# Kernel optimization log

Hardware: AMD Instinct MI355X
Metric: run time of the kernel (lower is better)

## Reference

```python
import jax, jax.numpy as jnp
import numpy as np

GROUPS = 32
EPS = 1e-6


def group_norm(x, gamma, beta):
    # x: [b, c, h, w], normalize over (c//GROUPS, h, w) within each group
    b, c, h, w = x.shape
    xg = x.reshape(b, GROUPS, c // GROUPS, h, w)
    mu = xg.mean(axis=(2, 3, 4), keepdims=True)
    var = xg.var(axis=(2, 3, 4), keepdims=True)
    xn = ((xg - mu) * jax.lax.rsqrt(var + EPS)).reshape(b, c, h, w)
    return xn * gamma[None, :, None, None] + beta[None, :, None, None]


def conv1x1(x, W, b):
    # 1x1 conv == channel GEMM. W: [out_c, in_c]
    return jnp.einsum('bchw,oc->bohw', x, W) + b[None, :, None, None]


def setup_inputs() -> dict:
    key = jax.random.key(0)
    ks = jax.random.split(key, 4)
    B, C, H, W = 4, 512, 64, 64
    wscale = 0.02
    return {
        'x': jax.random.normal(ks[0], (B, C, H, W), dtype=jnp.float32),
        'gn_w': jnp.ones((C,), dtype=jnp.float32),
        'gn_b': jnp.zeros((C,), dtype=jnp.float32),
        'q_w': jax.random.normal(ks[1], (C, C), dtype=jnp.float32) * wscale,
        'q_b': jnp.zeros((C,), dtype=jnp.float32),
        'k_w': jax.random.normal(ks[2], (C, C), dtype=jnp.float32) * wscale,
        'k_b': jnp.zeros((C,), dtype=jnp.float32),
        'v_w': jax.random.normal(ks[3], (C, C), dtype=jnp.float32) * wscale,
        'v_b': jnp.zeros((C,), dtype=jnp.float32),
    }


def reference(x, gn_w, gn_b, q_w, q_b, k_w, k_b, v_w, v_b):
    h_ = group_norm(x, gn_w, gn_b)
    q = conv1x1(h_, q_w, q_b)
    k = conv1x1(h_, k_w, k_b)
    v = conv1x1(h_, v_w, v_b)
    b, c, h, w = q.shape
    hw = h * w
    qf = q.reshape(b, c, hw)
    kf = k.reshape(b, c, hw)
    vf = v.reshape(b, c, hw)
    # attn[b, i, j] = sum_c q[b, c, i] * k[b, c, j] / sqrt(c)
    attn = jnp.einsum('bci,bcj->bij', qf, kf) * (c ** -0.5)
    attn = jax.nn.softmax(attn, axis=2)
    # A[b, c, i] = sum_j v[b, c, j] * attn[b, i, j]  (== bmm(v, attn^T))
    A = jnp.einsum('bcj,bij->bci', vf, attn).reshape(b, c, h, w)
    return x + A
```

## Files before the change

### kernel.cpp

```cpp
#include <hip/hip_runtime.h>
#include <hip/hip_bf16.h>

typedef __hip_bfloat16 bf16;
typedef __attribute__((ext_vector_type(8))) short short8;
typedef __attribute__((ext_vector_type(4))) float f32x4;
typedef __attribute__((ext_vector_type(8))) unsigned short u16x8;
typedef __attribute__((ext_vector_type(4))) unsigned short u16x4;

#define HWSZ 4096
#define CH 512
#define BATCH 4
#define NGROUPS 32
#define CPG 16
#define PER ((size_t)CH * HWSZ)

#define GLL16(gp, lp)                                                         \
  __builtin_amdgcn_global_load_lds(                                           \
      (const __attribute__((address_space(1))) void*)(gp),                    \
      (__attribute__((address_space(3))) void*)(lp), 16, 0, 0)

__device__ __forceinline__ float b2f(bf16 v) { return __bfloat162float(v); }
__device__ __forceinline__ bf16 f2b(float v) { return __float2bfloat16(v); }

__global__ void gn_part_kernel(const float* __restrict__ x, float2* __restrict__ gpart) {
  int bg = blockIdx.x >> 3, chunk = blockIdx.x & 7;
  size_t base = (size_t)bg * (CPG * HWSZ) + (size_t)chunk * 8192;
  int tid = threadIdx.x;
  float s = 0.f, ss = 0.f;
  const float4* xp = (const float4*)(x + base);
#pragma unroll
  for (int it = 0; it < 8; ++it) {
    float4 v = xp[tid + it * 256];
    s += v.x + v.y + v.z + v.w;
    ss += v.x * v.x + v.y * v.y + v.z * v.z + v.w * v.w;
  }
  __shared__ float rs[256], rss[256];
  rs[tid] = s; rss[tid] = ss;
  __syncthreads();
  for (int off = 128; off > 0; off >>= 1) {
    if (tid < off) { rs[tid] += rs[tid + off]; rss[tid] += rss[tid + off]; }
    __syncthreads();
  }
  if (tid == 0) gpart[blockIdx.x] = make_float2(rs[0], rss[0]);
}

__global__ void gn_final_kernel(const float2* __restrict__ gpart,
                                const float* __restrict__ gw, const float* __restrict__ gb,
                                float* __restrict__ sca, float* __restrict__ shf) {
  int idx = blockIdx.x * 256 + threadIdx.x;
  int b = idx >> 9, c = idx & 511;
  int bg = b * NGROUPS + (c >> 4);
  float s = 0.f, ss = 0.f;
#pragma unroll
  for (int t = 0; t < 8; ++t) {
    float2 p = gpart[bg * 8 + t];
    s += p.x; ss += p.y;
  }
  const float N = (float)(CPG * HWSZ);
  float mu = s / N;
  float var = ss / N - mu * mu;
  float inv = rsqrtf(var + 1e-6f);
  float a = inv * gw[c];
  sca[idx] = a;
  shf[idx] = gb[c] - mu * a;
}

__global__ void wconv_kernel(const float* __restrict__ qw, const float* __restrict__ kw,
                             const float* __restrict__ vw,
                             bf16* __restrict__ wq, bf16* __restrict__ wk, bf16* __restrict__ wv) {
  int i = blockIdx.x * 256 + threadIdx.x;
  wq[i] = f2b(qw[i]);
  wk[i] = f2b(kw[i]);
  wv[i] = f2b(vw[i]);
}

__global__ void h_apply_kernel(const float* __restrict__ x, const float* __restrict__ sca,
                               const float* __restrict__ shf, bf16* __restrict__ hT, int b0) {
  int p0 = blockIdx.x * 64, c0 = blockIdx.y * 64;
  int b = b0 + blockIdx.z;
  bf16* hTb = hT + (size_t)blockIdx.z * PER;
  __shared__ bf16 lt[64][66];
  int t = threadIdx.x;
  int pp = (t & 15) * 4, ccb = t >> 4;
#pragma unroll
  for (int it = 0; it < 4; ++it) {
    int cc = ccb + it * 16;
    int c = c0 + cc;
    float a = sca[b * CH + c], s = shf[b * CH + c];
    const float4 xv = *(const float4*)(x + ((size_t)(b * CH + c)) * HWSZ + p0 + pp);
    lt[cc][pp] = f2b(a * xv.x + s);
    lt[cc][pp + 1] = f2b(a * xv.y + s);
    lt[cc][pp + 2] = f2b(a * xv.z + s);
    lt[cc][pp + 3] = f2b(a * xv.w + s);
  }
  __syncthreads();
  int cc = (t & 15) * 4;
#pragma unroll
  for (int it = 0; it < 4; ++it) {
    int pr = (t >> 4) + it * 16;
    u16x4 o;
#pragma unroll
    for (int j = 0; j < 4; ++j) o[j] = *(const unsigned short*)&lt[cc + j][pr];
    *(u16x4*)(hTb + (size_t)(p0 + pr) * CH + c0 + cc) = o;
  }
}


__device__ __forceinline__ void mm_step(const bf16* la, const bf16* lb,
                                        f32x4 acc[4][4], int wm, int wn,
                                        int quad, int tm) {
#pragma unroll
  for (int kk = 0; kk < 2; ++kk) {
    const int go = ((kk * 4 + quad) ^ (tm & 7)) * 8;
    short8 aF[4], bF[4];
#pragma unroll
    for (int mt = 0; mt < 4; ++mt) {
      aF[mt] = *(const short8*)(la + (wm + mt * 16 + tm) * 64 + go);
      bF[mt] = *(const short8*)(lb + (wn + mt * 16 + tm) * 64 + go);
    }
#pragma unroll
    for (int mt = 0; mt < 4; ++mt)
#pragma unroll
      for (int nt = 0; nt < 4; ++nt)
        acc[mt][nt] = __builtin_amdgcn_mfma_f32_16x16x32_bf16(aF[mt], bF[nt],
                                                              acc[mt][nt], 0, 0, 0);
  }
}

#define MFMA_VARS()                                   \
  int tid = threadIdx.x;                              \
  int l = tid & 63, w = tid >> 6;                     \
  int quad = l >> 4, tm = l & 15;                     \
  int wm = (w & 1) * 64, wn = (w >> 1) * 64;          \
  int rr = l >> 3;                                    \
  int swz = ((l & 7) ^ rr) * 8;                       \
  bf16* stbase = smem + w * 2048

#define MSTAGE(bufsel, koff)                          \
  do {                                                \
    bf16* _d = stbase + (bufsel) * 16384;             \
    GLL16(sA0 + (koff), _d);                          \
    GLL16(sA1 + (koff), _d + 512);                    \
    GLL16(sA2 + (koff), _d + 1024);                   \
    GLL16(sA3 + (koff), _d + 1536);                   \
    GLL16(sB0 + (koff), _d + 8192);                   \
    GLL16(sB1 + (koff), _d + 8704);                   \
    GLL16(sB2 + (koff), _d + 9216);                   \
    GLL16(sB3 + (koff), _d + 9728);                   \
  } while (0)

#define MKLOOP(NS)                                                       \
  do {                                                                   \
    MSTAGE(0, 0);                                                        \
    for (int _t = 0; _t < (NS); ++_t) {                                  \
      if (_t + 1 < (NS)) {                                               \
        MSTAGE((_t + 1) & 1, (_t + 1) * 64);                             \
        asm volatile("s_waitcnt vmcnt(8)" ::: "memory");                 \
      } else {                                                           \
        asm volatile("s_waitcnt vmcnt(0)" ::: "memory");                 \
      }                                                                  \
      __builtin_amdgcn_s_barrier();                                      \
      mm_step(smem + (_t & 1) * 16384, smem + (_t & 1) * 16384 + 8192,   \
              acc, wm, wn, quad, tm);                                    \
      __builtin_amdgcn_s_barrier();                                      \
    }                                                                    \
  } while (0)

__global__ __launch_bounds__(256) void qkv_mfma(const bf16* __restrict__ hT,
                                                const bf16* __restrict__ wq,
                                                const bf16* __restrict__ wk,
                                                const bf16* __restrict__ wv,
                                                const float* __restrict__ qb,
                                                const float* __restrict__ kb,
                                                const float* __restrict__ vb,
                                                bf16* __restrict__ qT, bf16* __restrict__ kT,
                                                bf16* __restrict__ v) {
  int p0 = blockIdx.x * 128;
  int o0 = blockIdx.y * 128;
  int bz = blockIdx.z / 3, z = blockIdx.z % 3;
  const bf16* W = z == 0 ? wq : (z == 1 ? wk : wv);
  const float* bias = z == 0 ? qb : (z == 1 ? kb : vb);
  const bf16* hTb = hT + (size_t)bz * PER;
  __shared__ __align__(16) bf16 smem[32768];
  MFMA_VARS();
  const bf16* sA0 = hTb + (size_t)(p0 + w * 32 + rr) * CH + swz;
  const bf16* sA1 = sA0 + (size_t)8 * CH;
  const bf16* sA2 = sA0 + (size_t)16 * CH;
  const bf16* sA3 = sA0 + (size_t)24 * CH;
  const bf16* sB0 = W + (size_t)(o0 + w * 32 + rr) * CH + swz;
  const bf16* sB1 = sB0 + (size_t)8 * CH;
  const bf16* sB2 = sB0 + (size_t)16 * CH;
  const bf16* sB3 = sB0 + (size_t)24 * CH;
  f32x4 acc[4][4] = {};
  MKLOOP(CH / 64);
  if (z < 2) {
    bf16* outT = (z == 0 ? qT : kT) + (size_t)bz * PER;
#pragma unroll
    for (int nt = 0; nt < 4; ++nt) {
      int o = o0 + wn + nt * 16 + tm;
      float bv = bias[o];
#pragma unroll
      for (int mt = 0; mt < 4; ++mt)
#pragma unroll
        for (int r = 0; r < 4; ++r) {
          int p = p0 + wm + mt * 16 + quad * 4 + r;
          outT[(size_t)p * CH + o] = f2b(acc[mt][nt][r] + bv);
        }
    }
  } else {
    bf16* vv = v + (size_t)bz * PER;
    bf16* lt = smem;
    for (int chunk = 0; chunk < 2; ++chunk) {
      __syncthreads();
      if (wn == chunk * 64) {
#pragma unroll
        for (int nt = 0; nt < 4; ++nt) {
          int o = o0 + wn + nt * 16 + tm;
          float bv = bias[o];
#pragma unroll
          for (int mt = 0; mt < 4; ++mt)
#pragma unroll
            for (int r = 0; r < 4; ++r)
              lt[(nt * 16 + tm) * 136 + wm + mt * 16 + quad * 4 + r] = f2b(acc[mt][nt][r] + bv);
        }
      }
      __syncthreads();
      int oo = tid >> 2, ppb = (tid & 3) * 32;
      bf16* dst = vv + (size_t)(o0 + chunk * 64 + oo) * HWSZ + p0 + ppb;
      const bf16* src = lt + oo * 136 + ppb;
#pragma unroll
      for (int q4 = 0; q4 < 4; ++q4)
        *(u16x8*)(dst + q4 * 8) = *(const u16x8*)(src + q4 * 8);
    }
  }
}

__global__ __launch_bounds__(256) void s_mfma(const bf16* __restrict__ qT,
                                              const bf16* __restrict__ kT,
                                              bf16* __restrict__ attn,
                                              float* __restrict__ lsum) {
  int j0 = blockIdx.x * 128;
  int il0 = blockIdx.y * 128;
  int bz = blockIdx.z;
  const bf16* qTb = qT + (size_t)bz * PER;
  const bf16* kTb = kT + (size_t)bz * PER;
  bf16* attnb = attn + (size_t)bz * HWSZ * HWSZ;
  float* lsumb = lsum + (size_t)bz * HWSZ;
  __shared__ __align__(16) bf16 smem[32768];
  MFMA_VARS();
  const bf16* sA0 = qTb + (size_t)(il0 + w * 32 + rr) * CH + swz;
  const bf16* sA1 = sA0 + (size_t)8 * CH;
  const bf16* sA2 = sA0 + (size_t)16 * CH;
  const bf16* sA3 = sA0 + (size_t)24 * CH;
  const bf16* sB0 = kTb + (size_t)(j0 + w * 32 + rr) * CH + swz;
  const bf16* sB1 = sB0 + (size_t)8 * CH;
  const bf16* sB2 = sB0 + (size_t)16 * CH;
  const bf16* sB3 = sB0 + (size_t)24 * CH;
  f32x4 acc[4][4] = {};
  MKLOOP(CH / 64);
  const float scale = 0.044194173824159216f;
#pragma unroll
  for (int mt = 0; mt < 4; ++mt)
#pragma unroll
    for (int r = 0; r < 4; ++r) {
      int il = il0 + wm + mt * 16 + quad * 4 + r;
      float rs = 0.f;
#pragma unroll
      for (int nt = 0; nt < 4; ++nt) {
        float p = __expf(acc[mt][nt][r] * scale);
        rs += p;
        attnb[(size_t)il * HWSZ + j0 + wn + nt * 16 + tm] = f2b(p);
      }
      rs += __shfl_xor(rs, 1);
      rs += __shfl_xor(rs, 2);
      rs += __shfl_xor(rs, 4);
      rs += __shfl_xor(rs, 8);
      if (tm == 0) atomicAdd(&lsumb[il], rs);
    }
}

__global__ __launch_bounds__(256) void a_mfma(const bf16* __restrict__ v,
                                              const bf16* __restrict__ attn,
                                              float* __restrict__ acc_out,
                                              int KC, int ksplit) {
  int il0 = blockIdx.x * 128;
  int c00 = blockIdx.y * 128;
  int bz = blockIdx.z / ksplit;
  int kbase = (blockIdx.z % ksplit) * KC;
  const bf16* vb = v + (size_t)bz * PER;
  const bf16* attnb = attn + (size_t)bz * HWSZ * HWSZ;
  float* accb = acc_out + (size_t)bz * CH * HWSZ;
  __shared__ __align__(16) bf16 smem[32768];
  MFMA_VARS();
  const bf16* sA0 = vb + (size_t)(c00 + w * 32 + rr) * HWSZ + kbase + swz;
  const bf16* sA1 = sA0 + (size_t)8 * HWSZ;
  const bf16* sA2 = sA0 + (size_t)16 * HWSZ;
  const bf16* sA3 = sA0 + (size_t)24 * HWSZ;
  const bf16* sB0 = attnb + (size_t)(il0 + w * 32 + rr) * HWSZ + kbase + swz;
  const bf16* sB1 = sB0 + (size_t)8 * HWSZ;
  const bf16* sB2 = sB0 + (size_t)16 * HWSZ;
  const bf16* sB3 = sB0 + (size_t)24 * HWSZ;
  f32x4 acc[4][4] = {};
  MKLOOP(KC / 64);
#pragma unroll
  for (int mt = 0; mt < 4; ++mt)
#pragma unroll
    for (int nt = 0; nt < 4; ++nt)
#pragma unroll
      for (int r = 0; r < 4; ++r) {
        int c = c00 + wm + mt * 16 + quad * 4 + r;
        int il = il0 + wn + nt * 16 + tm;
        atomicAdd(&accb[(size_t)c * HWSZ + il], acc[mt][nt][r]);
      }
}

__global__ void add_kernel(const float* __restrict__ x, const float* __restrict__ acc,
                           const float* __restrict__ lsum, float* __restrict__ out, int b0) {
  int idx = blockIdx.x * 256 + threadIdx.x;
  int b = b0 + blockIdx.y;
  const float* accb = acc + (size_t)blockIdx.y * CH * HWSZ;
  const float* lsumb = lsum + (size_t)blockIdx.y * HWSZ;
  int c = idx >> 10;
  int r4 = (idx & 1023) * 4;
  size_t g = ((size_t)(b * CH + c)) * HWSZ + r4;
  const float4 xv = *(const float4*)(x + g);
  const float4 av = *(const float4*)(accb + (size_t)c * HWSZ + r4);
  const float4 lv = *(const float4*)(lsumb + r4);
  float4 o;
  o.x = xv.x + av.x / lv.x;
  o.y = xv.y + av.y / lv.y;
  o.z = xv.z + av.z / lv.z;
  o.w = xv.w + av.w / lv.w;
  *(float4*)(out + g) = o;
}

extern "C" void kernel_launch(void* const* d_in, const int* in_sizes, int n_in,
                              void* d_out, int out_size, void* d_ws, size_t ws_size,
                              hipStream_t stream) {
  const float* x   = (const float*)d_in[0];
  const float* gnw = (const float*)d_in[1];
  const float* gnb = (const float*)d_in[2];
  const float* qw  = (const float*)d_in[3];
  const float* qb  = (const float*)d_in[4];
  const float* kw  = (const float*)d_in[5];
  const float* kb  = (const float*)d_in[6];
  const float* vw  = (const float*)d_in[7];
  const float* vb  = (const float*)d_in[8];
  float* out = (float*)d_out;

  char* ws = (char*)d_ws;
  float* sca = (float*)ws;
  float* shf = sca + BATCH * CH;
  float2* gpart = (float2*)(ws + 16384);
  const size_t wsz = (size_t)CH * CH;
  bf16* wqb = (bf16*)(ws + 32768);
  bf16* wkb = wqb + wsz;
  bf16* wvb = wkb + wsz;
  char* dyn = (char*)(wvb + wsz);
  size_t base_used = (size_t)(dyn - ws);
  size_t perb = 4 * PER * sizeof(bf16) + (size_t)HWSZ * HWSZ * sizeof(bf16) +
                (size_t)CH * HWSZ * sizeof(float) + (size_t)HWSZ * sizeof(float);
  int nb = (int)(((long long)ws_size - (long long)base_used) / (long long)perb);
  if (nb < 1) nb = 1;
  if (nb > BATCH) nb = BATCH;
  bf16* hT = (bf16*)dyn;
  bf16* qT = hT + (size_t)nb * PER;
  bf16* kT = qT + (size_t)nb * PER;
  bf16* v  = kT + (size_t)nb * PER;
  bf16* attn = v + (size_t)nb * PER;
  float* acc = (float*)(attn + (size_t)nb * HWSZ * HWSZ);
  float* lsum = acc + (size_t)nb * CH * HWSZ;

  gn_part_kernel<<<dim3(BATCH * NGROUPS * 8), 256, 0, stream>>>(x, gpart);
  gn_final_kernel<<<dim3(8), 256, 0, stream>>>(gpart, gnw, gnb, sca, shf);
  wconv_kernel<<<dim3(wsz / 256), 256, 0, stream>>>(qw, kw, vw, wqb, wkb, wvb);
  for (int b0 = 0; b0 < BATCH; b0 += nb) {
    int nbc = BATCH - b0 < nb ? BATCH - b0 : nb;
    h_apply_kernel<<<dim3(HWSZ / 64, CH / 64, nbc), 256, 0, stream>>>(x, sca, shf, hT, b0);
    qkv_mfma<<<dim3(HWSZ / 128, CH / 128, 3 * nbc), 256, 0, stream>>>(hT, wqb, wkb, wvb,
                                                                      qb, kb, vb, qT, kT, v);
    hipMemsetAsync(acc, 0, (size_t)nbc * CH * HWSZ * sizeof(float), stream);
    hipMemsetAsync(lsum, 0, (size_t)nbc * HWSZ * sizeof(float), stream);
    int ksplit = 1024 / (32 * 4 * nbc);
    if (ksplit < 1) ksplit = 1;
    if (ksplit > 4) ksplit = 4;
    while (ksplit & (ksplit - 1)) --ksplit;
    int KC = HWSZ / ksplit;
    s_mfma<<<dim3(HWSZ / 128, HWSZ / 128, nbc), 256, 0, stream>>>(qT, kT, attn, lsum);
    a_mfma<<<dim3(HWSZ / 128, CH / 128, ksplit * nbc), 256, 0, stream>>>(v, attn, acc, KC, ksplit);
    add_kernel<<<dim3((CH * HWSZ) / 1024, nbc), 256, 0, stream>>>(x, acc, lsum, out, b0);
  }
}
```

Before: 352.5 us.

## Enlarge attention GEMM tiles to 256x256 with 8-wave blocks and phased MFMA loop

After: 367.6 us. +4.3%, slower.

```diff
diff --git a/kernel.cpp b/kernel.cpp
--- a/kernel.cpp
+++ b/kernel.cpp
@@ -164,6 +164,72 @@
               acc, wm, wn, quad, tm);                                    \
       __builtin_amdgcn_s_barrier();                                      \
     }                                                                    \
+  } while (0)
+
+
+#define MFMA_VARS256()                                \
+  int tid = threadIdx.x;                              \
+  int l = tid & 63, w = tid >> 6;                     \
+  int quad = l >> 4, tm = l & 15;                     \
+  int wm2 = (w & 1) * 128, wn2 = (w >> 1) * 64;       \
+  int rr = l >> 3;                                    \
+  int swz = ((l & 7) ^ rr) * 8
+
+#define MSTAGE256(bufsel, koff)                        \
+  do {                                                 \
+    bf16* _d = smem + (bufsel) * 32768 + w * 2048;     \
+    GLL16(sA0 + (koff), _d);                           \
+    GLL16(sA1 + (koff), _d + 512);                     \
+    GLL16(sA2 + (koff), _d + 1024);                    \
+    GLL16(sA3 + (koff), _d + 1536);                    \
+    GLL16(sB0 + (koff), _d + 16384);                   \
+    GLL16(sB1 + (koff), _d + 16896);                   \
+    GLL16(sB2 + (koff), _d + 17408);                   \
+    GLL16(sB3 + (koff), _d + 17920);                   \
+  } while (0)
+
+#define MKLOOP256(NS)                                                          \
+  do {                                                                         \
+    MSTAGE256(0, 0);                                                           \
+    asm volatile("s_waitcnt vmcnt(0)" ::: "memory");                           \
+    __builtin_amdgcn_s_barrier();                                              \
+    for (int _t = 0; _t < (NS); ++_t) {                                        \
+      const bf16* lA = smem + (_t & 1) * 32768;                                \
+      const bf16* lB = lA + 16384;                                             \
+      short8 bF[4];                                                            \
+      _Pragma("unroll")                                                        \
+      for (int ph = 0; ph < 4; ++ph) {                                         \
+        const int kk = ph >> 1, hh = ph & 1;                                   \
+        if (ph == 0 && _t + 1 < (NS)) MSTAGE256((_t + 1) & 1, (_t + 1) * 64);  \
+        if (hh == 0) {                                                         \
+          _Pragma("unroll")                                                    \
+          for (int nt = 0; nt < 4; ++nt) {                                     \
+            int rb = wn2 + nt * 16 + tm;                                       \
+            bF[nt] = *(const short8*)(lB + rb * 64 +                           \
+                                      (((kk * 4 + quad) ^ (rb & 7)) * 8));     \
+          }                                                                    \
+        }                                                                      \
+        short8 aF[4];                                                          \
+        _Pragma("unroll")                                                      \
+        for (int mt = 0; mt < 4; ++mt) {                                       \
+          int ra = wm2 + hh * 64 + mt * 16 + tm;                               \
+          aF[mt] = *(const short8*)(lA + ra * 64 +                             \
+                                    (((kk * 4 + quad) ^ (ra & 7)) * 8));       \
+        }                                                                      \
+        __builtin_amdgcn_s_barrier();                                          \
+        __builtin_amdgcn_s_setprio(1);                                         \
+        _Pragma("unroll")                                                      \
+        for (int mt = 0; mt < 4; ++mt)                                         \
+          _Pragma("unroll")                                                    \
+          for (int nt = 0; nt < 4; ++nt)                                       \
+            acc[hh * 4 + mt][nt] = __builtin_amdgcn_mfma_f32_16x16x32_bf16(    \
+                aF[mt], bF[nt], acc[hh * 4 + mt][nt], 0, 0, 0);                \
+        __builtin_amdgcn_s_setprio(0);                                         \
+        if (ph == 3 && _t + 1 < (NS))                                          \
+          asm volatile("s_waitcnt vmcnt(0)" ::: "memory");                     \
+        __builtin_amdgcn_s_barrier();                                          \
+      }                                                                        \
+    }                                                                          \
   } while (0)
 
 __global__ __launch_bounds__(256) void qkv_mfma(const bf16* __restrict__ hT,
@@ -235,19 +301,19 @@
   }
 }
 
-__global__ __launch_bounds__(256) void s_mfma(const bf16* __restrict__ qT,
-                                              const bf16* __restrict__ kT,
-                                              bf16* __restrict__ attn,
-                                              float* __restrict__ lsum) {
-  int j0 = blockIdx.x * 128;
-  int il0 = blockIdx.y * 128;
+__global__ __launch_bounds__(512, 2) void s_mfma(const bf16* __restrict__ qT,
+                                                 const bf16* __restrict__ kT,
+                                                 bf16* __restrict__ attn,
+                                                 float* __restrict__ lsum) {
+  int j0 = blockIdx.x * 256;
+  int il0 = blockIdx.y * 256;
   int bz = blockIdx.z;
   const bf16* qTb = qT + (size_t)bz * PER;
   const bf16* kTb = kT + (size_t)bz * PER;
   bf16* attnb = attn + (size_t)bz * HWSZ * HWSZ;
   float* lsumb = lsum + (size_t)bz * HWSZ;
-  __shared__ __align__(16) bf16 smem[32768];
-  MFMA_VARS();
+  __shared__ __align__(16) bf16 smem[65536];
+  MFMA_VARS256();
   const bf16* sA0 = qTb + (size_t)(il0 + w * 32 + rr) * CH + swz;
   const bf16* sA1 = sA0 + (size_t)8 * CH;
   const bf16* sA2 = sA0 + (size_t)16 * CH;
@@ -256,20 +322,20 @@
   const bf16* sB1 = sB0 + (size_t)8 * CH;
   const bf16* sB2 = sB0 + (size_t)16 * CH;
   const bf16* sB3 = sB0 + (size_t)24 * CH;
-  f32x4 acc[4][4] = {};
-  MKLOOP(CH / 64);
+  f32x4 acc[8][4] = {};
+  MKLOOP256(CH / 64);
   const float scale = 0.044194173824159216f;
 #pragma unroll
-  for (int mt = 0; mt < 4; ++mt)
+  for (int m8 = 0; m8 < 8; ++m8)
 #pragma unroll
     for (int r = 0; r < 4; ++r) {
-      int il = il0 + wm + mt * 16 + quad * 4 + r;
+      int il = il0 + wm2 + m8 * 16 + quad * 4 + r;
       float rs = 0.f;
 #pragma unroll
       for (int nt = 0; nt < 4; ++nt) {
-        float p = __expf(acc[mt][nt][r] * scale);
+        float p = __expf(acc[m8][nt][r] * scale);
         rs += p;
-        attnb[(size_t)il * HWSZ + j0 + wn + nt * 16 + tm] = f2b(p);
+        attnb[(size_t)il * HWSZ + j0 + wn2 + nt * 16 + tm] = f2b(p);
       }
       rs += __shfl_xor(rs, 1);
       rs += __shfl_xor(rs, 2);
@@ -279,19 +345,19 @@
     }
 }
 
-__global__ __launch_bounds__(256) void a_mfma(const bf16* __restrict__ v,
-                                              const bf16* __restrict__ attn,
-                                              float* __restrict__ acc_out,
-                                              int KC, int ksplit) {
-  int il0 = blockIdx.x * 128;
-  int c00 = blockIdx.y * 128;
+__global__ __launch_bounds__(512, 2) void a_mfma(const bf16* __restrict__ v,
+                                                 const bf16* __restrict__ attn,
+                                                 float* __restrict__ acc_out,
+                                                 int KC, int ksplit) {
+  int il0 = blockIdx.x * 256;
+  int c00 = blockIdx.y * 256;
   int bz = blockIdx.z / ksplit;
   int kbase = (blockIdx.z % ksplit) * KC;
   const bf16* vb = v + (size_t)bz * PER;
   const bf16* attnb = attn + (size_t)bz * HWSZ * HWSZ;
   float* accb = acc_out + (size_t)bz * CH * HWSZ;
-  __shared__ __align__(16) bf16 smem[32768];
-  MFMA_VARS();
+  __shared__ __align__(16) bf16 smem[65536];
+  MFMA_VARS256();
   const bf16* sA0 = vb + (size_t)(c00 + w * 32 + rr) * HWSZ + kbase + swz;
   const bf16* sA1 = sA0 + (size_t)8 * HWSZ;
   const bf16* sA2 = sA0 + (size_t)16 * HWSZ;
@@ -300,17 +366,17 @@
   const bf16* sB1 = sB0 + (size_t)8 * HWSZ;
   const bf16* sB2 = sB0 + (size_t)16 * HWSZ;
   const bf16* sB3 = sB0 + (size_t)24 * HWSZ;
-  f32x4 acc[4][4] = {};
-  MKLOOP(KC / 64);
-#pragma unroll
-  for (int mt = 0; mt < 4; ++mt)
+  f32x4 acc[8][4] = {};
+  MKLOOP256(KC / 64);
+#pragma unroll
+  for (int m8 = 0; m8 < 8; ++m8)
 #pragma unroll
     for (int nt = 0; nt < 4; ++nt)
 #pragma unroll
       for (int r = 0; r < 4; ++r) {
-        int c = c00 + wm + mt * 16 + quad * 4 + r;
-        int il = il0 + wn + nt * 16 + tm;
-        atomicAdd(&accb[(size_t)c * HWSZ + il], acc[mt][nt][r]);
+        int c = c00 + wm2 + m8 * 16 + quad * 4 + r;
+        int il = il0 + wn2 + nt * 16 + tm;
+        atomicAdd(&accb[(size_t)c * HWSZ + il], acc[m8][nt][r]);
       }
 }
 
@@ -381,13 +447,13 @@
                                                                       qb, kb, vb, qT, kT, v);
     hipMemsetAsync(acc, 0, (size_t)nbc * CH * HWSZ * sizeof(float), stream);
     hipMemsetAsync(lsum, 0, (size_t)nbc * HWSZ * sizeof(float), stream);
-    int ksplit = 1024 / (32 * 4 * nbc);
+    int ksplit = 256 / (16 * (CH / 256) * nbc);
     if (ksplit < 1) ksplit = 1;
     if (ksplit > 4) ksplit = 4;
     while (ksplit & (ksplit - 1)) --ksplit;
     int KC = HWSZ / ksplit;
-    s_mfma<<<dim3(HWSZ / 128, HWSZ / 128, nbc), 256, 0, stream>>>(qT, kT, attn, lsum);
-    a_mfma<<<dim3(HWSZ / 128, CH / 128, ksplit * nbc), 256, 0, stream>>>(v, attn, acc, KC, ksplit);
+    s_mfma<<<dim3(HWSZ / 256, HWSZ / 256, nbc), 512, 0, stream>>>(qT, kT, attn, lsum);
+    a_mfma<<<dim3(HWSZ / 256, CH / 256, ksplit * nbc), 512, 0, stream>>>(v, attn, acc, KC, ksplit);
     add_kernel<<<dim3((CH * HWSZ) / 1024, nbc), 256, 0, stream>>>(x, acc, lsum, out, b0);
   }
 }
```
